# Kernel tuning notes

Measured on AMD Instinct MI355X. Metric: run time of the kernel, lower is better.

The kernel has to match this reference:

```python
import jax, jax.numpy as jnp
import numpy as np

EPS = 1e-5


def gcn_conv(x, src, dst, n_nodes, W, b):
    # x: [B, N, Fin]; src/dst: [E+N] (self loops included); W: [Fout, Fin]
    h = jnp.einsum('bnf,of->bno', x, W)                      # [B, N, Fout]
    deg = jnp.zeros((n_nodes,), h.dtype).at[dst].add(1.0)    # in-degree of A+I
    dinv = jnp.where(deg > 0, 1.0 / jnp.sqrt(deg), 0.0)
    norm = dinv[src] * dinv[dst]                             # [E+N]
    msg = h[:, src, :] * norm[None, :, None]                 # gather along node axis
    out = jnp.zeros_like(h).at[:, dst, :].add(msg)           # scatter-add aggregate
    return out + b


def batchnorm_nodes(x, gamma, beta):
    # torch BatchNorm1d(N) on [B, N, C]: channel axis is N, stats over (B, C)
    mean = jnp.mean(x, axis=(0, 2), keepdims=True)
    var = jnp.mean(jnp.square(x - mean), axis=(0, 2), keepdims=True)
    xn = (x - mean) * jax.lax.rsqrt(var + EPS)
    return xn * gamma[None, :, None] + beta[None, :, None]


def setup_inputs() -> dict:
    key = jax.random.key(0)
    ks = jax.random.split(key, 20)
    B, N, FIN, D, OUT, E = 4096, 64, 67, 2048, 2, 512
    s = 0.1
    d = {}
    d['x_fingerprints'] = jax.random.normal(ks[0], (B, D), jnp.float32)
    d['x_node_features'] = jax.random.normal(ks[1], (B, N, FIN), jnp.float32)
    d['edge_list'] = jax.random.randint(ks[2], (2, E), 0, N)
    d['W1'] = jax.random.normal(ks[3], (64, FIN), jnp.float32) * s
    d['b1'] = jax.random.normal(ks[4], (64,), jnp.float32) * s
    d['g1'] = 1.0 + jax.random.normal(ks[5], (N,), jnp.float32) * s
    d['be1'] = jax.random.normal(ks[6], (N,), jnp.float32) * s
    d['W2'] = jax.random.normal(ks[7], (32, 64), jnp.float32) * s
    d['b2'] = jax.random.normal(ks[8], (32,), jnp.float32) * s
    d['g2'] = 1.0 + jax.random.normal(ks[9], (N,), jnp.float32) * s
    d['be2'] = jax.random.normal(ks[10], (N,), jnp.float32) * s
    d['Wl1'] = jax.random.normal(ks[11], (400, D), jnp.float32) * (s / 4)
    d['bl1'] = jax.random.normal(ks[12], (400,), jnp.float32) * s
    d['Wl2'] = jax.random.normal(ks[13], (64, 400), jnp.float32) * s
    d['bl2'] = jax.random.normal(ks[14], (64,), jnp.float32) * s
    d['Wfc'] = jax.random.normal(ks[15], (OUT, 96), jnp.float32) * s
    d['bfc'] = jax.random.normal(ks[16], (OUT,), jnp.float32) * s
    return d


def reference(x_fingerprints, x_node_features, edge_list, W1, b1, g1, be1,
              W2, b2, g2, be2, Wl1, bl1, Wl2, bl2, Wfc, bfc):
    B, N, _ = x_node_features.shape
    loops = jnp.arange(N)
    src = jnp.concatenate([edge_list[0], loops])  # add self loops (GCNConv default)
    dst = jnp.concatenate([edge_list[1], loops])
    g = gcn_conv(x_node_features, src, dst, N, W1, b1)
    g = jax.nn.relu(batchnorm_nodes(g, g1, be1))
    g = gcn_conv(g, src, dst, N, W2, b2)
    g = jax.nn.relu(batchnorm_nodes(g, g2, be2))           # [B, N, 32]
    pooled = jnp.max(g, axis=1)                             # global_max_pool -> [B, 32]
    h = jax.nn.relu(x_fingerprints @ Wl1.T + bl1)
    h = jax.nn.relu(h @ Wl2.T + bl2)                        # [B, 64]
    out = jnp.concatenate([pooled, h], axis=1) @ Wfc.T + bfc
    return out
```

## Files before the change

### kernel.cpp

```cpp
#include <hip/hip_runtime.h>
#include <hip/hip_bf16.h>
#include <math.h>

typedef __bf16 bf16;
typedef __attribute__((ext_vector_type(8))) __bf16 bf16x8;
typedef __attribute__((ext_vector_type(4))) __bf16 bf16x4;
typedef __attribute__((ext_vector_type(4))) float f32x4;

#define EPSBN 1e-5f
#define NSLOT 128

__global__ __launch_bounds__(256) void k0_prep(const int* __restrict__ edge,
    const float* __restrict__ W1, const float* __restrict__ W2,
    float* __restrict__ partials,
    bf16* __restrict__ ahb,
    bf16* __restrict__ w1b,
    bf16* __restrict__ w2b)
{
    int tid = threadIdx.x;
    for (int i = blockIdx.x * 256 + tid; i < NSLOT * 64 * 4; i += gridDim.x * 256)
        partials[i] = 0.f;
    if (blockIdx.x == 1) {
        for (int i = tid; i < 64 * 104; i += 256) {
            int n = i / 104, f = i % 104;
            w1b[i] = (bf16)((f < 67) ? W1[n * 67 + f] : 0.f);
        }
        return;
    }
    if (blockIdx.x == 2) {
        for (int i = tid; i < 32 * 72; i += 256) {
            int n = i / 72, f = i % 72;
            w2b[i] = (bf16)((f < 64) ? W2[n * 64 + f] : 0.f);
        }
        return;
    }
    if (blockIdx.x != 0) return;

    __shared__ float Ah[64 * 64];
    __shared__ int deg[64];
    __shared__ float dinv[64];
    for (int i = tid; i < 4096; i += 256) Ah[i] = 0.f;
    if (tid < 64) deg[tid] = 1;
    __syncthreads();
    for (int e = tid; e < 512; e += 256) atomicAdd(&deg[edge[512 + e]], 1);
    __syncthreads();
    if (tid < 64) dinv[tid] = rsqrtf((float)deg[tid]);
    __syncthreads();
    for (int e = tid; e < 512; e += 256) {
        int s = edge[e], d = edge[512 + e];
        atomicAdd(&Ah[d * 64 + s], dinv[s] * dinv[d]);
    }
    if (tid < 64) atomicAdd(&Ah[tid * 64 + tid], dinv[tid] * dinv[tid]);
    __syncthreads();
    for (int i = tid; i < 64 * 72; i += 256) {
        int n = i / 72, s = i % 72;
        ahb[i] = (bf16)((s < 64) ? Ah[n * 64 + s] : 0.f);
    }
}

__global__ __launch_bounds__(256) void k1_gcn1(
    const float* __restrict__ x,
    const bf16* __restrict__ w1b,
    const bf16* __restrict__ ahb,
    const float* __restrict__ b1,
    bf16* __restrict__ g1out,
    float* __restrict__ part1)
{
    __shared__ bf16 sW[64 * 104];
    __shared__ bf16 sX[4 * 64 * 104];
    __shared__ bf16 sAh[64 * 72];
    __shared__ float sstat[128];
    int tid = threadIdx.x;
    int blk = blockIdx.x;
    if (tid < 128) sstat[tid] = 0.f;

#pragma unroll
    for (int k = 0; k < 4; ++k) {
        int c = tid + (k << 8);
        if (c < 832) ((bf16x8*)sW)[c] = ((const bf16x8*)w1b)[c];
    }
#pragma unroll
    for (int k = 0; k < 3; ++k) {
        int c = tid + (k << 8);
        if (c < 576) ((bf16x8*)sAh)[c] = ((const bf16x8*)ahb)[c];
    }
    const float* xb = x + (size_t)blk * 17152;
    for (int k = 0; k < 67; ++k) {
        int j = tid + (k << 8);
        int s = j / 4288, r = j % 4288;
        int n = r / 67, f = r % 67;
        sX[s * 6656 + n * 104 + f] = (bf16)xb[j];
    }
    for (int k = 0; k < 29; ++k) {
        int j = tid + (k << 8);
        int s = j / 1856, r = j % 1856;
        int n = r / 29, f = 67 + r % 29;
        sX[s * 6656 + n * 104 + f] = (bf16)0.f;
    }
    __syncthreads();

    int w = tid >> 6, lane = tid & 63, q = lane >> 4, r15 = lane & 15;
    bf16* myX = sX + w * 6656;
    f32x4 z4 = {0.f, 0.f, 0.f, 0.f};
    f32x4 acc[4][4];
#pragma unroll
    for (int mt = 0; mt < 4; ++mt)
#pragma unroll
        for (int nt = 0; nt < 4; ++nt) acc[mt][nt] = z4;
#pragma unroll
    for (int kt = 0; kt < 3; ++kt) {
        bf16x8 a_[4], b_[4];
#pragma unroll
        for (int mt = 0; mt < 4; ++mt)
            a_[mt] = *(const bf16x8*)&sW[(mt * 16 + r15) * 104 + kt * 32 + q * 8];
#pragma unroll
        for (int nt = 0; nt < 4; ++nt)
            b_[nt] = *(const bf16x8*)&myX[(nt * 16 + r15) * 104 + kt * 32 + q * 8];
#pragma unroll
        for (int mt = 0; mt < 4; ++mt)
#pragma unroll
            for (int nt = 0; nt < 4; ++nt)
                acc[mt][nt] = __builtin_amdgcn_mfma_f32_16x16x32_bf16(a_[mt], b_[nt], acc[mt][nt], 0, 0, 0);
    }
#pragma unroll
    for (int mt = 0; mt < 4; ++mt)
#pragma unroll
        for (int nt = 0; nt < 4; ++nt)
#pragma unroll
            for (int r = 0; r < 4; ++r)
                myX[(mt * 16 + q * 4 + r) * 104 + nt * 16 + r15] = (bf16)acc[mt][nt][r];

    bf16x8 ah[4][2], hb[4][2];
#pragma unroll
    for (int mt = 0; mt < 4; ++mt)
#pragma unroll
        for (int kt = 0; kt < 2; ++kt)
            ah[mt][kt] = *(const bf16x8*)&sAh[(mt * 16 + r15) * 72 + kt * 32 + q * 8];
#pragma unroll
    for (int ct = 0; ct < 4; ++ct)
#pragma unroll
        for (int kt = 0; kt < 2; ++kt)
            hb[ct][kt] = *(const bf16x8*)&myX[(ct * 16 + r15) * 104 + kt * 32 + q * 8];

    f32x4 o2[4][4];
#pragma unroll
    for (int mt = 0; mt < 4; ++mt)
#pragma unroll
        for (int ct = 0; ct < 4; ++ct) o2[mt][ct] = z4;
#pragma unroll
    for (int kt = 0; kt < 2; ++kt)
#pragma unroll
        for (int mt = 0; mt < 4; ++mt)
#pragma unroll
            for (int ct = 0; ct < 4; ++ct)
                o2[mt][ct] = __builtin_amdgcn_mfma_f32_16x16x32_bf16(ah[mt][kt], hb[ct][kt], o2[mt][ct], 0, 0, 0);

    float bv[4];
#pragma unroll
    for (int ct = 0; ct < 4; ++ct) bv[ct] = b1[ct * 16 + r15];
#pragma unroll
    for (int mt = 0; mt < 4; ++mt)
#pragma unroll
        for (int ct = 0; ct < 4; ++ct)
#pragma unroll
            for (int r = 0; r < 4; ++r)
                myX[(mt * 16 + q * 4 + r) * 72 + ct * 16 + r15] = (bf16)(o2[mt][ct][r] + bv[ct]);
    __syncthreads();

    bf16* gp = g1out + (size_t)blk * 16384;
#pragma unroll
    for (int k = 0; k < 8; ++k) {
        int c = tid + (k << 8);
        int s = c >> 9, rc = c & 511, n = rc >> 3, cc = rc & 7;
        bf16x8 v = *(const bf16x8*)&sX[s * 6656 + n * 72 + cc * 8];
        ((bf16x8*)gp)[c] = v;
        float s1 = 0.f, s2 = 0.f;
#pragma unroll
        for (int j = 0; j < 8; ++j) { float f = (float)v[j]; s1 += f; s2 += f * f; }
        atomicAdd(&sstat[n * 2 + 0], s1);
        atomicAdd(&sstat[n * 2 + 1], s2);
    }
    __syncthreads();
    if (tid < 64) {
        int slot = blk & (NSLOT - 1);
        atomicAdd(&part1[(slot * 64 + tid) * 2 + 0], sstat[tid * 2 + 0]);
        atomicAdd(&part1[(slot * 64 + tid) * 2 + 1], sstat[tid * 2 + 1]);
    }
}

__global__ __launch_bounds__(64) void k_bnstats(
    const float* __restrict__ part,
    const float* __restrict__ gamma, const float* __restrict__ beta,
    float* __restrict__ scale, float* __restrict__ shift, float inv_count)
{
    int n = blockIdx.x, t = threadIdx.x;
    float s1 = part[(t * 64 + n) * 2] + part[((t + 64) * 64 + n) * 2];
    float s2 = part[(t * 64 + n) * 2 + 1] + part[((t + 64) * 64 + n) * 2 + 1];
#pragma unroll
    for (int o = 32; o > 0; o >>= 1) { s1 += __shfl_down(s1, o); s2 += __shfl_down(s2, o); }
    if (t == 0) {
        float mean = s1 * inv_count;
        float var = s2 * inv_count - mean * mean;
        float sc = gamma[n] * rsqrtf(var + EPSBN);
        scale[n] = sc;
        shift[n] = beta[n] - mean * sc;
    }
}

__global__ __launch_bounds__(256) void k3_gcn2(
    const bf16* __restrict__ g1out,
    const bf16* __restrict__ w2b,
    const bf16* __restrict__ ahb,
    const float* __restrict__ b2,
    const float* __restrict__ scale1, const float* __restrict__ shift1,
    bf16* __restrict__ g2out,
    float* __restrict__ part2)
{
    __shared__ bf16 sW[32 * 72];
    __shared__ bf16 sY[4 * 64 * 72];
    __shared__ bf16 sAh[64 * 72];
    __shared__ float sstat[128];
    __shared__ float ssc[64], ssh[64];
    int tid = threadIdx.x;
    int blk = blockIdx.x;
    if (tid < 128) sstat[tid] = 0.f;
    if (tid < 64) { ssc[tid] = scale1[tid]; ssh[tid] = shift1[tid]; }
#pragma unroll
    for (int k = 0; k < 2; ++k) {
        int c = tid + (k << 8);
        if (c < 288) ((bf16x8*)sW)[c] = ((const bf16x8*)w2b)[c];
    }
#pragma unroll
    for (int k = 0; k < 3; ++k) {
        int c = tid + (k << 8);
        if (c < 576) ((bf16x8*)sAh)[c] = ((const bf16x8*)ahb)[c];
    }
    __syncthreads();

    const bf16* gb = g1out + (size_t)blk * 16384;
#pragma unroll
    for (int k = 0; k < 8; ++k) {
        int c = tid + (k << 8);
        int s = c >> 9, rc = c & 511, n = rc >> 3, cc = rc & 7;
        bf16x8 g = ((const bf16x8*)gb)[c];
        float sc = ssc[n], sh = ssh[n];
        bf16x8 y;
#pragma unroll
        for (int j = 0; j < 8; ++j)
            y[j] = (bf16)fmaxf(fmaf(sc, (float)g[j], sh), 0.f);
        *(bf16x8*)&sY[s * 4608 + n * 72 + cc * 8] = y;
    }
    __syncthreads();

    int w = tid >> 6, lane = tid & 63, q = lane >> 4, r15 = lane & 15;
    bf16* myY = sY + w * 4608;
    f32x4 z4 = {0.f, 0.f, 0.f, 0.f};
    f32x4 acc[2][4];
#pragma unroll
    for (int mt = 0; mt < 2; ++mt)
#pragma unroll
        for (int nt = 0; nt < 4; ++nt) acc[mt][nt] = z4;
#pragma unroll
    for (int kt = 0; kt < 2; ++kt) {
        bf16x8 a_[2], b_[4];
#pragma unroll
        for (int mt = 0; mt < 2; ++mt)
            a_[mt] = *(const bf16x8*)&sW[(mt * 16 + r15) * 72 + kt * 32 + q * 8];
#pragma unroll
        for (int nt = 0; nt < 4; ++nt)
            b_[nt] = *(const bf16x8*)&myY[(nt * 16 + r15) * 72 + kt * 32 + q * 8];
#pragma unroll
        for (int mt = 0; mt < 2; ++mt)
#pragma unroll
            for (int nt = 0; nt < 4; ++nt)
                acc[mt][nt] = __builtin_amdgcn_mfma_f32_16x16x32_bf16(a_[mt], b_[nt], acc[mt][nt], 0, 0, 0);
    }
#pragma unroll
    for (int mt = 0; mt < 2; ++mt)
#pragma unroll
        for (int nt = 0; nt < 4; ++nt)
#pragma unroll
            for (int r = 0; r < 4; ++r)
                myY[(mt * 16 + q * 4 + r) * 72 + nt * 16 + r15] = (bf16)acc[mt][nt][r];

    bf16x8 ah[4][2], hb[2][2];
#pragma unroll
    for (int mt = 0; mt < 4; ++mt)
#pragma unroll
        for (int kt = 0; kt < 2; ++kt)
            ah[mt][kt] = *(const bf16x8*)&sAh[(mt * 16 + r15) * 72 + kt * 32 + q * 8];
#pragma unroll
    for (int ct = 0; ct < 2; ++ct)
#pragma unroll
        for (int kt = 0; kt < 2; ++kt)
            hb[ct][kt] = *(const bf16x8*)&myY[(ct * 16 + r15) * 72 + kt * 32 + q * 8];

    f32x4 o2[4][2];
#pragma unroll
    for (int mt = 0; mt < 4; ++mt)
#pragma unroll
        for (int ct = 0; ct < 2; ++ct) o2[mt][ct] = z4;
#pragma unroll
    for (int kt = 0; kt < 2; ++kt)
#pragma unroll
        for (int mt = 0; mt < 4; ++mt)
#pragma unroll
            for (int ct = 0; ct < 2; ++ct)
                o2[mt][ct] = __builtin_amdgcn_mfma_f32_16x16x32_bf16(ah[mt][kt], hb[ct][kt], o2[mt][ct], 0, 0, 0);

    float bv[2];
#pragma unroll
    for (int ct = 0; ct < 2; ++ct) bv[ct] = b2[ct * 16 + r15];
#pragma unroll
    for (int mt = 0; mt < 4; ++mt)
#pragma unroll
        for (int ct = 0; ct < 2; ++ct)
#pragma unroll
            for (int r = 0; r < 4; ++r)
                myY[(mt * 16 + q * 4 + r) * 40 + ct * 16 + r15] = (bf16)(o2[mt][ct][r] + bv[ct]);
    __syncthreads();

    bf16* gp = g2out + (size_t)blk * 8192;
#pragma unroll
    for (int k = 0; k < 4; ++k) {
        int c = tid + (k << 8);
        int s = c >> 8, rc = c & 255, n = rc >> 2, cc = rc & 3;
        bf16x8 v = *(const bf16x8*)&sY[s * 4608 + n * 40 + cc * 8];
        ((bf16x8*)gp)[c] = v;
        float s1 = 0.f, s2 = 0.f;
#pragma unroll
        for (int j = 0; j < 8; ++j) { float f = (float)v[j]; s1 += f; s2 += f * f; }
        atomicAdd(&sstat[n * 2 + 0], s1);
        atomicAdd(&sstat[n * 2 + 1], s2);
    }
    __syncthreads();
    if (tid < 64) {
        int slot = blk & (NSLOT - 1);
        atomicAdd(&part2[(slot * 64 + tid) * 2 + 0], sstat[tid * 2 + 0]);
        atomicAdd(&part2[(slot * 64 + tid) * 2 + 1], sstat[tid * 2 + 1]);
    }
}

__global__ __launch_bounds__(256) void k6_mlp1(
    const float* __restrict__ A,
    const float* __restrict__ Bw,
    float* __restrict__ part)
{
    __shared__ bf16 As[64 * 36];
    __shared__ bf16 Bs[64 * 36];
    int tid = threadIdx.x;
    int m0 = blockIdx.x * 64, n0 = blockIdx.y * 64, ks = blockIdx.z;
    int row = tid >> 2, seg = tid & 3;
    int w = tid >> 6, lane = tid & 63, q = lane >> 4, r15 = lane & 15;
    f32x4 z4 = {0.f, 0.f, 0.f, 0.f};
    f32x4 acc[4] = {z4, z4, z4, z4};
    const float* pA = A + (size_t)(m0 + row) * 2048 + ks * 512 + seg * 8;
    bool bvalid = (n0 + row) < 400;
    const float* pB = Bw + (size_t)(n0 + row) * 2048 + ks * 512 + seg * 8;

    f32x4 a0 = *(const f32x4*)pA;
    f32x4 a1 = *(const f32x4*)(pA + 4);
    f32x4 c0 = z4, c1 = z4;
    if (bvalid) { c0 = *(const f32x4*)pB; c1 = *(const f32x4*)(pB + 4); }

    for (int kt = 0; kt < 16; ++kt) {
        bf16x8 apk, bpk;
        apk[0] = (bf16)a0[0]; apk[1] = (bf16)a0[1]; apk[2] = (bf16)a0[2]; apk[3] = (bf16)a0[3];
        apk[4] = (bf16)a1[0]; apk[5] = (bf16)a1[1]; apk[6] = (bf16)a1[2]; apk[7] = (bf16)a1[3];
        bpk[0] = (bf16)c0[0]; bpk[1] = (bf16)c0[1]; bpk[2] = (bf16)c0[2]; bpk[3] = (bf16)c0[3];
        bpk[4] = (bf16)c1[0]; bpk[5] = (bf16)c1[1]; bpk[6] = (bf16)c1[2]; bpk[7] = (bf16)c1[3];
        __syncthreads();
        *(bf16x8*)&As[row * 36 + seg * 8] = apk;
        *(bf16x8*)&Bs[row * 36 + seg * 8] = bpk;
        __syncthreads();
        if (kt < 15) {
            pA += 32; pB += 32;
            a0 = *(const f32x4*)pA; a1 = *(const f32x4*)(pA + 4);
            if (bvalid) { c0 = *(const f32x4*)pB; c1 = *(const f32x4*)(pB + 4); }
        }
        bf16x8 a = *(const bf16x8*)&As[(w * 16 + r15) * 36 + q * 8];
#pragma unroll
        for (int nt = 0; nt < 4; ++nt) {
            bf16x8 bb = *(const bf16x8*)&Bs[(nt * 16 + r15) * 36 + q * 8];
            acc[nt] = __builtin_amdgcn_mfma_f32_16x16x32_bf16(a, bb, acc[nt], 0, 0, 0);
        }
    }
    float* pp = part + (size_t)ks * 1638400;
#pragma unroll
    for (int nt = 0; nt < 4; ++nt)
#pragma unroll
        for (int r = 0; r < 4; ++r) {
            int mm = m0 + w * 16 + q * 4 + r;
            int nn = n0 + nt * 16 + r15;
            if (nn < 400) pp[(size_t)mm * 400 + nn] = acc[nt][r];
        }
}

__global__ __launch_bounds__(256) void k6_reduce(
    const float* __restrict__ part,
    const float* __restrict__ bias,
    bf16* __restrict__ h1)
{
    int i = blockIdx.x * 256 + threadIdx.x;
    const f32x4* p = (const f32x4*)part;
    f32x4 s0 = p[i], s1v = p[i + 409600], s2v = p[i + 819200], s3v = p[i + 1228800];
    int nn = (i * 4) % 400;
    f32x4 bv = *(const f32x4*)&bias[nn];
    bf16x4 ov;
    ov[0] = (bf16)fmaxf(s0[0] + s1v[0] + s2v[0] + s3v[0] + bv[0], 0.f);
    ov[1] = (bf16)fmaxf(s0[1] + s1v[1] + s2v[1] + s3v[1] + bv[1], 0.f);
    ov[2] = (bf16)fmaxf(s0[2] + s1v[2] + s2v[2] + s3v[2] + bv[2], 0.f);
    ov[3] = (bf16)fmaxf(s0[3] + s1v[3] + s2v[3] + s3v[3] + bv[3], 0.f);
    *(bf16x4*)&h1[i * 4] = ov;
}

__global__ __launch_bounds__(256) void k7_mlp2(
    const bf16* __restrict__ A,
    const float* __restrict__ Bw,
    const float* __restrict__ bias,
    float* __restrict__ Cout)
{
    __shared__ bf16 As[16 * 416];
    int tid = threadIdx.x;
    int m0 = blockIdx.x * 16;
    for (int i = tid; i < 16 * 50; i += 256) {
        int rr = i / 50, cc = (i % 50) * 8;
        *(bf16x8*)&As[rr * 416 + cc] = *(const bf16x8*)(A + (size_t)(m0 + rr) * 400 + cc);
    }
    if (tid < 32) {
        int rr = tid >> 1, cc = 400 + (tid & 1) * 8;
        bf16x8 z;
#pragma unroll
        for (int k = 0; k < 8; ++k) z[k] = (bf16)0.f;
        *(bf16x8*)&As[rr * 416 + cc] = z;
    }
    __syncthreads();

    int w = tid >> 6, lane = tid & 63, q = lane >> 4, r15 = lane & 15;
    f32x4 acc = {0.f, 0.f, 0.f, 0.f};
    const float* pB = Bw + (size_t)(w * 16 + r15) * 400;
#pragma unroll 4
    for (int kt = 0; kt < 13; ++kt) {
        int k0 = kt * 32 + q * 8;
        bf16x8 a = *(const bf16x8*)&As[r15 * 416 + k0];
        bf16x8 bb;
#pragma unroll
        for (int k = 0; k < 8; ++k) bb[k] = (bf16)0.f;
        if (k0 < 400) {
            f32x4 c0 = *(const f32x4*)(pB + k0);
            f32x4 c1 = *(const f32x4*)(pB + k0 + 4);
            bb[0] = (bf16)c0[0]; bb[1] = (bf16)c0[1]; bb[2] = (bf16)c0[2]; bb[3] = (bf16)c0[3];
            bb[4] = (bf16)c1[0]; bb[5] = (bf16)c1[1]; bb[6] = (bf16)c1[2]; bb[7] = (bf16)c1[3];
        }
        acc = __builtin_amdgcn_mfma_f32_16x16x32_bf16(a, bb, acc, 0, 0, 0);
    }
#pragma unroll
    for (int r = 0; r < 4; ++r) {
        int mm = m0 + q * 4 + r;
        int nn = w * 16 + r15;
        float v = fmaxf(acc[r] + bias[nn], 0.f);
        Cout[(size_t)mm * 64 + nn] = v;
    }
}

__global__ __launch_bounds__(256) void k8_final(
    const bf16* __restrict__ g2out,
    const float* __restrict__ scale2, const float* __restrict__ shift2,
    const float* __restrict__ h2,
    const float* __restrict__ Wfc,
    const float* __restrict__ bfc,
    float* __restrict__ out)
{
    __shared__ float s2s[64], sh2s[64];
    int tid = threadIdx.x;
    if (tid < 64) { s2s[tid] = scale2[tid]; sh2s[tid] = shift2[tid]; }
    __syncthreads();
    int w = tid >> 6, lane = tid & 63;
    int b = blockIdx.x * 4 + w;
    int c = lane & 31, half = lane >> 5;
    const bf16* gb = g2out + (size_t)b * 2048;
    float mx = 0.f;
    for (int i = 0; i < 32; ++i) {
        int n = half * 32 + i;
        float v = (float)gb[n * 32 + c];
        float val = fmaf(s2s[n], v, sh2s[n]);
        mx = fmaxf(mx, val);
    }
    mx = fmaxf(mx, __shfl_xor(mx, 32));
    float h2v = h2[(size_t)b * 64 + lane];
#pragma unroll
    for (int o = 0; o < 2; ++o) {
        float t = h2v * Wfc[o * 96 + 32 + lane];
        if (half == 0) t += mx * Wfc[o * 96 + c];
#pragma unroll
        for (int off = 32; off > 0; off >>= 1) t += __shfl_xor(t, off);
        if (lane == 0) out[(size_t)b * 2 + o] = t + bfc[o];
    }
}

extern "C" void kernel_launch(void* const* d_in, const int* in_sizes, int n_in,
                              void* d_out, int out_size, void* d_ws, size_t ws_size,
                              hipStream_t stream)
{
    const float* x_fp   = (const float*)d_in[0];
    const float* x_node = (const float*)d_in[1];
    const int*   edge   = (const int*)d_in[2];
    const float* W1     = (const float*)d_in[3];
    const float* b1     = (const float*)d_in[4];
    const float* g1     = (const float*)d_in[5];
    const float* be1    = (const float*)d_in[6];
    const float* W2     = (const float*)d_in[7];
    const float* b2     = (const float*)d_in[8];
    const float* g2     = (const float*)d_in[9];
    const float* be2    = (const float*)d_in[10];
    const float* Wl1    = (const float*)d_in[11];
    const float* bl1    = (const float*)d_in[12];
    const float* Wl2    = (const float*)d_in[13];
    const float* bl2    = (const float*)d_in[14];
    const float* Wfc    = (const float*)d_in[15];
    const float* bfc    = (const float*)d_in[16];
    float* out = (float*)d_out;

    char* ws = (char*)d_ws;
    bf16*  w1b     = (bf16*)(ws);
    bf16*  ahb     = (bf16*)(ws + 13312);
    bf16*  w2b     = (bf16*)(ws + 22528);
    float* scale1  = (float*)(ws + 27136);
    float* shift1  = (float*)(ws + 27392);
    float* scale2  = (float*)(ws + 27648);
    float* shift2  = (float*)(ws + 27904);
    float* part1   = (float*)(ws + 28672);
    float* part2   = (float*)(ws + 94208);
    bf16*  g1out   = (bf16*)(ws + 159744);
    float* part6   = (float*)(ws + 159744);
    bf16*  g2out   = (bf16*)(ws + 33714176ull);
    bf16*  h1      = (bf16*)(ws + 50491392ull);
    float* h2      = (float*)(ws + 53768192ull);

    k0_prep<<<dim3(16), dim3(256), 0, stream>>>(edge, W1, W2, part1, ahb, w1b, w2b);
    k1_gcn1<<<dim3(1024), dim3(256), 0, stream>>>(x_node, w1b, ahb, b1, g1out, part1);
    k_bnstats<<<dim3(64), dim3(64), 0, stream>>>(part1, g1, be1, scale1, shift1,
                                                 1.f / (4096.f * 64.f));
    k3_gcn2<<<dim3(1024), dim3(256), 0, stream>>>(g1out, w2b, ahb, b2, scale1, shift1,
                                                  g2out, part2);
    k_bnstats<<<dim3(64), dim3(64), 0, stream>>>(part2, g2, be2, scale2, shift2,
                                                 1.f / (4096.f * 32.f));
    k6_mlp1<<<dim3(64, 7, 4), dim3(256), 0, stream>>>(x_fp, Wl1, part6);
    k6_reduce<<<dim3(1600), dim3(256), 0, stream>>>(part6, bl1, h1);
    k7_mlp2<<<dim3(256), dim3(256), 0, stream>>>(h1, Wl2, bl2, h2);
    k8_final<<<dim3(1024), dim3(256), 0, stream>>>(g2out, scale2, shift2, h2, Wfc, bfc, out);
}
```

Measured before the change: 285.9 us.

## Pre-convert node features to padded bf16 and split GCN1 into chunked launches

Adds a conversion kernel that turns fp32 node features into a padded bf16 layout in quarter-batch chunks, each followed by a GCN1 launch. GCN1 now handles two samples per block, splitting each sample's work across two waves, and loads its tile with vector copies instead of scalar strided conversion. The aim is to remove the slow scattered fp32-to-bf16 staging and cut shared memory per block to raise occupancy. In exchange it adds an extra global round trip for the converted input, eight launches instead of one, and extra block barriers.

New measurement: 338.5 us. +18.4%, slower.

```diff
diff --git a/kernel.cpp b/kernel.cpp
--- a/kernel.cpp
+++ b/kernel.cpp
@@ -58,22 +58,50 @@
     }
 }
 
+__global__ __launch_bounds__(256) void kx_conv(const float* __restrict__ x,
+    bf16* __restrict__ xbq, int s0)
+{
+    int tid = threadIdx.x;
+    const float* xs = x + ((size_t)s0 + blockIdx.x * 2) * 4288;
+    bf16* xo = xbq + (size_t)blockIdx.x * 13312;
+#pragma unroll
+    for (int k = 0; k < 7; ++k) {
+        int c = tid + (k << 8);
+        if (c < 1664) {
+            int ls = c >> 9 >= 1 ? (c >= 832) : (c >= 832);
+            ls = (c >= 832) ? 1 : 0;
+            int cc = c - ls * 832;
+            int n = cc / 13;
+            int seg = cc - n * 13;
+            int f0 = seg * 8;
+            const float* src = xs + ls * 4288 + n * 67 + f0;
+            bf16x8 v;
+#pragma unroll
+            for (int j = 0; j < 8; ++j) {
+                float t = (f0 + j < 67) ? src[j] : 0.f;
+                v[j] = (bf16)t;
+            }
+            *(bf16x8*)(xo + (size_t)c * 8) = v;
+        }
+    }
+}
+
 __global__ __launch_bounds__(256) void k1_gcn1(
-    const float* __restrict__ x,
+    const bf16* __restrict__ xbq,
     const bf16* __restrict__ w1b,
     const bf16* __restrict__ ahb,
     const float* __restrict__ b1,
     bf16* __restrict__ g1out,
-    float* __restrict__ part1)
+    float* __restrict__ part1,
+    int s0)
 {
     __shared__ bf16 sW[64 * 104];
-    __shared__ bf16 sX[4 * 64 * 104];
+    __shared__ bf16 sX[2 * 64 * 104];
     __shared__ bf16 sAh[64 * 72];
     __shared__ float sstat[128];
     int tid = threadIdx.x;
     int blk = blockIdx.x;
     if (tid < 128) sstat[tid] = 0.f;
-
 #pragma unroll
     for (int k = 0; k < 4; ++k) {
         int c = tid + (k << 8);
@@ -84,73 +112,71 @@
         int c = tid + (k << 8);
         if (c < 576) ((bf16x8*)sAh)[c] = ((const bf16x8*)ahb)[c];
     }
-    const float* xb = x + (size_t)blk * 17152;
-    for (int k = 0; k < 67; ++k) {
-        int j = tid + (k << 8);
-        int s = j / 4288, r = j % 4288;
-        int n = r / 67, f = r % 67;
-        sX[s * 6656 + n * 104 + f] = (bf16)xb[j];
-    }
-    for (int k = 0; k < 29; ++k) {
-        int j = tid + (k << 8);
-        int s = j / 1856, r = j % 1856;
-        int n = r / 29, f = 67 + r % 29;
-        sX[s * 6656 + n * 104 + f] = (bf16)0.f;
+    const bf16x8* xp = (const bf16x8*)(xbq + (size_t)blk * 13312);
+#pragma unroll
+    for (int k = 0; k < 7; ++k) {
+        int c = tid + (k << 8);
+        if (c < 1664) ((bf16x8*)sX)[c] = xp[c];
     }
     __syncthreads();
 
     int w = tid >> 6, lane = tid & 63, q = lane >> 4, r15 = lane & 15;
-    bf16* myX = sX + w * 6656;
+    int sm = w >> 1, hw = w & 1;
+    bf16* myX = sX + sm * 6656;
     f32x4 z4 = {0.f, 0.f, 0.f, 0.f};
-    f32x4 acc[4][4];
-#pragma unroll
-    for (int mt = 0; mt < 4; ++mt)
+    f32x4 acc[2][4];
+#pragma unroll
+    for (int mt = 0; mt < 2; ++mt)
 #pragma unroll
         for (int nt = 0; nt < 4; ++nt) acc[mt][nt] = z4;
 #pragma unroll
     for (int kt = 0; kt < 3; ++kt) {
-        bf16x8 a_[4], b_[4];
-#pragma unroll
-        for (int mt = 0; mt < 4; ++mt)
-            a_[mt] = *(const bf16x8*)&sW[(mt * 16 + r15) * 104 + kt * 32 + q * 8];
+        bf16x8 a_[2], b_[4];
+#pragma unroll
+        for (int mt = 0; mt < 2; ++mt)
+            a_[mt] = *(const bf16x8*)&sW[((hw * 2 + mt) * 16 + r15) * 104 + kt * 32 + q * 8];
 #pragma unroll
         for (int nt = 0; nt < 4; ++nt)
             b_[nt] = *(const bf16x8*)&myX[(nt * 16 + r15) * 104 + kt * 32 + q * 8];
 #pragma unroll
-        for (int mt = 0; mt < 4; ++mt)
+        for (int mt = 0; mt < 2; ++mt)
 #pragma unroll
             for (int nt = 0; nt < 4; ++nt)
                 acc[mt][nt] = __builtin_amdgcn_mfma_f32_16x16x32_bf16(a_[mt], b_[nt], acc[mt][nt], 0, 0, 0);
     }
-#pragma unroll
-    for (int mt = 0; mt < 4; ++mt)
+    __syncthreads();
+#pragma unroll
+    for (int mt = 0; mt < 2; ++mt)
 #pragma unroll
         for (int nt = 0; nt < 4; ++nt)
 #pragma unroll
             for (int r = 0; r < 4; ++r)
-                myX[(mt * 16 + q * 4 + r) * 104 + nt * 16 + r15] = (bf16)acc[mt][nt][r];
-
-    bf16x8 ah[4][2], hb[4][2];
-#pragma unroll
-    for (int mt = 0; mt < 4; ++mt)
+                myX[((hw * 2 + mt) * 16 + q * 4 + r) * 104 + nt * 16 + r15] = (bf16)acc[mt][nt][r];
+
+    bf16x8 ah[2][2];
+#pragma unroll
+    for (int mt = 0; mt < 2; ++mt)
 #pragma unroll
         for (int kt = 0; kt < 2; ++kt)
-            ah[mt][kt] = *(const bf16x8*)&sAh[(mt * 16 + r15) * 72 + kt * 32 + q * 8];
+            ah[mt][kt] = *(const bf16x8*)&sAh[((hw * 2 + mt) * 16 + r15) * 72 + kt * 32 + q * 8];
+    __syncthreads();
+
+    bf16x8 hb[4][2];
 #pragma unroll
     for (int ct = 0; ct < 4; ++ct)
 #pragma unroll
         for (int kt = 0; kt < 2; ++kt)
             hb[ct][kt] = *(const bf16x8*)&myX[(ct * 16 + r15) * 104 + kt * 32 + q * 8];
 
-    f32x4 o2[4][4];
-#pragma unroll
-    for (int mt = 0; mt < 4; ++mt)
+    f32x4 o2[2][4];
+#pragma unroll
+    for (int mt = 0; mt < 2; ++mt)
 #pragma unroll
         for (int ct = 0; ct < 4; ++ct) o2[mt][ct] = z4;
 #pragma unroll
     for (int kt = 0; kt < 2; ++kt)
 #pragma unroll
-        for (int mt = 0; mt < 4; ++mt)
+        for (int mt = 0; mt < 2; ++mt)
 #pragma unroll
             for (int ct = 0; ct < 4; ++ct)
                 o2[mt][ct] = __builtin_amdgcn_mfma_f32_16x16x32_bf16(ah[mt][kt], hb[ct][kt], o2[mt][ct], 0, 0, 0);
@@ -158,18 +184,19 @@
     float bv[4];
 #pragma unroll
     for (int ct = 0; ct < 4; ++ct) bv[ct] = b1[ct * 16 + r15];
-#pragma unroll
-    for (int mt = 0; mt < 4; ++mt)
+    __syncthreads();
+#pragma unroll
+    for (int mt = 0; mt < 2; ++mt)
 #pragma unroll
         for (int ct = 0; ct < 4; ++ct)
 #pragma unroll
             for (int r = 0; r < 4; ++r)
-                myX[(mt * 16 + q * 4 + r) * 72 + ct * 16 + r15] = (bf16)(o2[mt][ct][r] + bv[ct]);
-    __syncthreads();
-
-    bf16* gp = g1out + (size_t)blk * 16384;
-#pragma unroll
-    for (int k = 0; k < 8; ++k) {
+                myX[((hw * 2 + mt) * 16 + q * 4 + r) * 72 + ct * 16 + r15] = (bf16)(o2[mt][ct][r] + bv[ct]);
+    __syncthreads();
+
+    bf16* gp = g1out + ((size_t)s0 + blk * 2) * 4096;
+#pragma unroll
+    for (int k = 0; k < 4; ++k) {
         int c = tid + (k << 8);
         int s = c >> 9, rc = c & 511, n = rc >> 3, cc = rc & 7;
         bf16x8 v = *(const bf16x8*)&sX[s * 6656 + n * 72 + cc * 8];
@@ -182,7 +209,7 @@
     }
     __syncthreads();
     if (tid < 64) {
-        int slot = blk & (NSLOT - 1);
+        int slot = (s0 + blk * 2) & (NSLOT - 1);
         atomicAdd(&part1[(slot * 64 + tid) * 2 + 0], sstat[tid * 2 + 0]);
         atomicAdd(&part1[(slot * 64 + tid) * 2 + 1], sstat[tid * 2 + 1]);
     }
@@ -531,14 +558,20 @@
     float* shift2  = (float*)(ws + 27904);
     float* part1   = (float*)(ws + 28672);
     float* part2   = (float*)(ws + 94208);
-    bf16*  g1out   = (bf16*)(ws + 159744);
-    float* part6   = (float*)(ws + 159744);
-    bf16*  g2out   = (bf16*)(ws + 33714176ull);
-    bf16*  h1      = (bf16*)(ws + 50491392ull);
-    float* h2      = (float*)(ws + 53768192ull);
+    char*  pool    = ws + 196608;
+    bf16*  g1out   = (bf16*)(pool);
+    float* part6   = (float*)(pool);
+    float* h2      = (float*)(pool + 26214400);
+    bf16*  xbq     = (bf16*)(pool + 33554432);
+    bf16*  g2out   = (bf16*)(pool + 33554432);
+    bf16*  h1      = (bf16*)(pool + 50331648);
 
     k0_prep<<<dim3(16), dim3(256), 0, stream>>>(edge, W1, W2, part1, ahb, w1b, w2b);
-    k1_gcn1<<<dim3(1024), dim3(256), 0, stream>>>(x_node, w1b, ahb, b1, g1out, part1);
+    for (int qtr = 0; qtr < 4; ++qtr) {
+        int s0 = qtr * 1024;
+        kx_conv<<<dim3(512), dim3(256), 0, stream>>>(x_node, xbq, s0);
+        k1_gcn1<<<dim3(512), dim3(256), 0, stream>>>(xbq, w1b, ahb, b1, g1out, part1, s0);
+    }
     k_bnstats<<<dim3(64), dim3(64), 0, stream>>>(part1, g1, be1, scale1, shift1,
                                                  1.f / (4096.f * 64.f));
     k3_gcn2<<<dim3(1024), dim3(256), 0, stream>>>(g1out, w2b, ahb, b2, scale1, shift1,
```

## Process one graph per block in GCN kernels, splitting matmul tiles across waves

Applied to the files above, without the earlier changes.

The two GCN kernels now handle a single graph per 256-thread block, with the four waves splitting the output row tiles, instead of each wave owning a whole graph. Grid size grows from 1024 to 4096 blocks. Weight and adjacency fragments are loaded straight from global memory into registers, and node features are staged with vectorized float4 loads before the bf16 conversion. The intent is to cut LDS use and register pressure for higher occupancy and better-coalesced input loads. The cost is more blocks, extra barriers between stages, and the workspace layout is rearranged so part6 no longer aliases g1out.

Measured after the change: 275.0 us. 3.8% less time.

```diff
diff --git a/kernel.cpp b/kernel.cpp
--- a/kernel.cpp
+++ b/kernel.cpp
@@ -66,113 +66,98 @@
     bf16* __restrict__ g1out,
     float* __restrict__ part1)
 {
-    __shared__ bf16 sW[64 * 104];
-    __shared__ bf16 sX[4 * 64 * 104];
-    __shared__ bf16 sAh[64 * 72];
+    __shared__ float sXf[4288];
+    __shared__ bf16 sX[64 * 104];
     __shared__ float sstat[128];
     int tid = threadIdx.x;
     int blk = blockIdx.x;
     if (tid < 128) sstat[tid] = 0.f;
 
-#pragma unroll
-    for (int k = 0; k < 4; ++k) {
+    const f32x4* xp = (const f32x4*)(x + (size_t)blk * 4288);
+#pragma unroll
+    for (int k = 0; k < 5; ++k) {
         int c = tid + (k << 8);
-        if (c < 832) ((bf16x8*)sW)[c] = ((const bf16x8*)w1b)[c];
-    }
-#pragma unroll
-    for (int k = 0; k < 3; ++k) {
+        if (c < 1072) ((f32x4*)sXf)[c] = xp[c];
+    }
+
+    int w = tid >> 6, lane = tid & 63, q = lane >> 4, r15 = lane & 15;
+    bf16x8 aw[3], ah[2];
+#pragma unroll
+    for (int kt = 0; kt < 3; ++kt)
+        aw[kt] = *(const bf16x8*)&w1b[(w * 16 + r15) * 104 + kt * 32 + q * 8];
+#pragma unroll
+    for (int kt = 0; kt < 2; ++kt)
+        ah[kt] = *(const bf16x8*)&ahb[(w * 16 + r15) * 72 + kt * 32 + q * 8];
+    __syncthreads();
+
+    {
+        int n = tid & 63, sg = tid >> 6;
+#pragma unroll
+        for (int i = 0; i < 4; ++i) {
+            int seg = sg + 4 * i;
+            if (seg < 13) {
+                int f0 = seg * 8;
+                bf16x8 v;
+#pragma unroll
+                for (int j = 0; j < 8; ++j) {
+                    int f = f0 + j;
+                    float t = (f < 67) ? sXf[n * 67 + f] : 0.f;
+                    v[j] = (bf16)t;
+                }
+                *(bf16x8*)&sX[n * 104 + f0] = v;
+            }
+        }
+    }
+    __syncthreads();
+
+    f32x4 z4 = {0.f, 0.f, 0.f, 0.f};
+    f32x4 acc[4] = {z4, z4, z4, z4};
+#pragma unroll
+    for (int kt = 0; kt < 3; ++kt) {
+        bf16x8 b_[4];
+#pragma unroll
+        for (int nt = 0; nt < 4; ++nt)
+            b_[nt] = *(const bf16x8*)&sX[(nt * 16 + r15) * 104 + kt * 32 + q * 8];
+#pragma unroll
+        for (int nt = 0; nt < 4; ++nt)
+            acc[nt] = __builtin_amdgcn_mfma_f32_16x16x32_bf16(aw[kt], b_[nt], acc[nt], 0, 0, 0);
+    }
+    __syncthreads();
+#pragma unroll
+    for (int nt = 0; nt < 4; ++nt)
+#pragma unroll
+        for (int r = 0; r < 4; ++r)
+            sX[(w * 16 + q * 4 + r) * 104 + nt * 16 + r15] = (bf16)acc[nt][r];
+    __syncthreads();
+
+    f32x4 o2[4] = {z4, z4, z4, z4};
+#pragma unroll
+    for (int kt = 0; kt < 2; ++kt) {
+        bf16x8 hbv[4];
+#pragma unroll
+        for (int ct = 0; ct < 4; ++ct)
+            hbv[ct] = *(const bf16x8*)&sX[(ct * 16 + r15) * 104 + kt * 32 + q * 8];
+#pragma unroll
+        for (int ct = 0; ct < 4; ++ct)
+            o2[ct] = __builtin_amdgcn_mfma_f32_16x16x32_bf16(ah[kt], hbv[ct], o2[ct], 0, 0, 0);
+    }
+    float bv[4];
+#pragma unroll
+    for (int ct = 0; ct < 4; ++ct) bv[ct] = b1[ct * 16 + r15];
+    __syncthreads();
+#pragma unroll
+    for (int ct = 0; ct < 4; ++ct)
+#pragma unroll
+        for (int r = 0; r < 4; ++r)
+            sX[(w * 16 + q * 4 + r) * 72 + ct * 16 + r15] = (bf16)(o2[ct][r] + bv[ct]);
+    __syncthreads();
+
+    bf16* gp = g1out + (size_t)blk * 4096;
+#pragma unroll
+    for (int k = 0; k < 2; ++k) {
         int c = tid + (k << 8);
-        if (c < 576) ((bf16x8*)sAh)[c] = ((const bf16x8*)ahb)[c];
-    }
-    const float* xb = x + (size_t)blk * 17152;
-    for (int k = 0; k < 67; ++k) {
-        int j = tid + (k << 8);
-        int s = j / 4288, r = j % 4288;
-        int n = r / 67, f = r % 67;
-        sX[s * 6656 + n * 104 + f] = (bf16)xb[j];
-    }
-    for (int k = 0; k < 29; ++k) {
-        int j = tid + (k << 8);
-        int s = j / 1856, r = j % 1856;
-        int n = r / 29, f = 67 + r % 29;
-        sX[s * 6656 + n * 104 + f] = (bf16)0.f;
-    }
-    __syncthreads();
-
-    int w = tid >> 6, lane = tid & 63, q = lane >> 4, r15 = lane & 15;
-    bf16* myX = sX + w * 6656;
-    f32x4 z4 = {0.f, 0.f, 0.f, 0.f};
-    f32x4 acc[4][4];
-#pragma unroll
-    for (int mt = 0; mt < 4; ++mt)
-#pragma unroll
-        for (int nt = 0; nt < 4; ++nt) acc[mt][nt] = z4;
-#pragma unroll
-    for (int kt = 0; kt < 3; ++kt) {
-        bf16x8 a_[4], b_[4];
-#pragma unroll
-        for (int mt = 0; mt < 4; ++mt)
-            a_[mt] = *(const bf16x8*)&sW[(mt * 16 + r15) * 104 + kt * 32 + q * 8];
-#pragma unroll
-        for (int nt = 0; nt < 4; ++nt)
-            b_[nt] = *(const bf16x8*)&myX[(nt * 16 + r15) * 104 + kt * 32 + q * 8];
-#pragma unroll
-        for (int mt = 0; mt < 4; ++mt)
-#pragma unroll
-            for (int nt = 0; nt < 4; ++nt)
-                acc[mt][nt] = __builtin_amdgcn_mfma_f32_16x16x32_bf16(a_[mt], b_[nt], acc[mt][nt], 0, 0, 0);
-    }
-#pragma unroll
-    for (int mt = 0; mt < 4; ++mt)
-#pragma unroll
-        for (int nt = 0; nt < 4; ++nt)
-#pragma unroll
-            for (int r = 0; r < 4; ++r)
-                myX[(mt * 16 + q * 4 + r) * 104 + nt * 16 + r15] = (bf16)acc[mt][nt][r];
-
-    bf16x8 ah[4][2], hb[4][2];
-#pragma unroll
-    for (int mt = 0; mt < 4; ++mt)
-#pragma unroll
-        for (int kt = 0; kt < 2; ++kt)
-            ah[mt][kt] = *(const bf16x8*)&sAh[(mt * 16 + r15) * 72 + kt * 32 + q * 8];
-#pragma unroll
-    for (int ct = 0; ct < 4; ++ct)
-#pragma unroll
-        for (int kt = 0; kt < 2; ++kt)
-            hb[ct][kt] = *(const bf16x8*)&myX[(ct * 16 + r15) * 104 + kt * 32 + q * 8];
-
-    f32x4 o2[4][4];
-#pragma unroll
-    for (int mt = 0; mt < 4; ++mt)
-#pragma unroll
-        for (int ct = 0; ct < 4; ++ct) o2[mt][ct] = z4;
-#pragma unroll
-    for (int kt = 0; kt < 2; ++kt)
-#pragma unroll
-        for (int mt = 0; mt < 4; ++mt)
-#pragma unroll
-            for (int ct = 0; ct < 4; ++ct)
-                o2[mt][ct] = __builtin_amdgcn_mfma_f32_16x16x32_bf16(ah[mt][kt], hb[ct][kt], o2[mt][ct], 0, 0, 0);
-
-    float bv[4];
-#pragma unroll
-    for (int ct = 0; ct < 4; ++ct) bv[ct] = b1[ct * 16 + r15];
-#pragma unroll
-    for (int mt = 0; mt < 4; ++mt)
-#pragma unroll
-        for (int ct = 0; ct < 4; ++ct)
-#pragma unroll
-            for (int r = 0; r < 4; ++r)
-                myX[(mt * 16 + q * 4 + r) * 72 + ct * 16 + r15] = (bf16)(o2[mt][ct][r] + bv[ct]);
-    __syncthreads();
-
-    bf16* gp = g1out + (size_t)blk * 16384;
-#pragma unroll
-    for (int k = 0; k < 8; ++k) {
-        int c = tid + (k << 8);
-        int s = c >> 9, rc = c & 511, n = rc >> 3, cc = rc & 7;
-        bf16x8 v = *(const bf16x8*)&sX[s * 6656 + n * 72 + cc * 8];
+        int n = c >> 3, cc = c & 7;
+        bf16x8 v = *(const bf16x8*)&sX[n * 72 + cc * 8];
         ((bf16x8*)gp)[c] = v;
         float s1 = 0.f, s2 = 0.f;
 #pragma unroll
@@ -216,116 +201,85 @@
     bf16* __restrict__ g2out,
     float* __restrict__ part2)
 {
-    __shared__ bf16 sW[32 * 72];
-    __shared__ bf16 sY[4 * 64 * 72];
-    __shared__ bf16 sAh[64 * 72];
+    __shared__ bf16 sY[64 * 72];
+    __shared__ bf16 sH[32 * 72];
+    __shared__ bf16 sO[64 * 40];
+    __shared__ float ssc[64], ssh[64];
     __shared__ float sstat[128];
-    __shared__ float ssc[64], ssh[64];
     int tid = threadIdx.x;
     int blk = blockIdx.x;
     if (tid < 128) sstat[tid] = 0.f;
     if (tid < 64) { ssc[tid] = scale1[tid]; ssh[tid] = shift1[tid]; }
+
+    int w = tid >> 6, lane = tid & 63, q = lane >> 4, r15 = lane & 15;
+    bf16x8 aw[2][2], ah[2];
+#pragma unroll
+    for (int mt = 0; mt < 2; ++mt)
+#pragma unroll
+        for (int kt = 0; kt < 2; ++kt)
+            aw[mt][kt] = *(const bf16x8*)&w2b[(mt * 16 + r15) * 72 + kt * 32 + q * 8];
+#pragma unroll
+    for (int kt = 0; kt < 2; ++kt)
+        ah[kt] = *(const bf16x8*)&ahb[(w * 16 + r15) * 72 + kt * 32 + q * 8];
+    __syncthreads();
+
+    const bf16* gb = g1out + (size_t)blk * 4096;
 #pragma unroll
     for (int k = 0; k < 2; ++k) {
         int c = tid + (k << 8);
-        if (c < 288) ((bf16x8*)sW)[c] = ((const bf16x8*)w2b)[c];
-    }
-#pragma unroll
-    for (int k = 0; k < 3; ++k) {
-        int c = tid + (k << 8);
-        if (c < 576) ((bf16x8*)sAh)[c] = ((const bf16x8*)ahb)[c];
-    }
-    __syncthreads();
-
-    const bf16* gb = g1out + (size_t)blk * 16384;
-#pragma unroll
-    for (int k = 0; k < 8; ++k) {
-        int c = tid + (k << 8);
-        int s = c >> 9, rc = c & 511, n = rc >> 3, cc = rc & 7;
+        int n = c >> 3, cc = c & 7;
         bf16x8 g = ((const bf16x8*)gb)[c];
         float sc = ssc[n], sh = ssh[n];
         bf16x8 y;
 #pragma unroll
         for (int j = 0; j < 8; ++j)
             y[j] = (bf16)fmaxf(fmaf(sc, (float)g[j], sh), 0.f);
-        *(bf16x8*)&sY[s * 4608 + n * 72 + cc * 8] = y;
-    }
-    __syncthreads();
-
-    int w = tid >> 6, lane = tid & 63, q = lane >> 4, r15 = lane & 15;
-    bf16* myY = sY + w * 4608;
+        *(bf16x8*)&sY[n * 72 + cc * 8] = y;
+    }
+    __syncthreads();
+
     f32x4 z4 = {0.f, 0.f, 0.f, 0.f};
-    f32x4 acc[2][4];
+    f32x4 acc[2] = {z4, z4};
+#pragma unroll
+    for (int kt = 0; kt < 2; ++kt) {
+        bf16x8 b_ = *(const bf16x8*)&sY[(w * 16 + r15) * 72 + kt * 32 + q * 8];
+#pragma unroll
+        for (int mt = 0; mt < 2; ++mt)
+            acc[mt] = __builtin_amdgcn_mfma_f32_16x16x32_bf16(aw[mt][kt], b_, acc[mt], 0, 0, 0);
+    }
 #pragma unroll
     for (int mt = 0; mt < 2; ++mt)
 #pragma unroll
-        for (int nt = 0; nt < 4; ++nt) acc[mt][nt] = z4;
+        for (int r = 0; r < 4; ++r)
+            sH[(mt * 16 + q * 4 + r) * 72 + w * 16 + r15] = (bf16)acc[mt][r];
+    __syncthreads();
+
+    f32x4 o2[2] = {z4, z4};
 #pragma unroll
     for (int kt = 0; kt < 2; ++kt) {
-        bf16x8 a_[2], b_[4];
-#pragma unroll
-        for (int mt = 0; mt < 2; ++mt)
-            a_[mt] = *(const bf16x8*)&sW[(mt * 16 + r15) * 72 + kt * 32 + q * 8];
-#pragma unroll
-        for (int nt = 0; nt < 4; ++nt)
-            b_[nt] = *(const bf16x8*)&myY[(nt * 16 + r15) * 72 + kt * 32 + q * 8];
-#pragma unroll
-        for (int mt = 0; mt < 2; ++mt)
-#pragma unroll
-            for (int nt = 0; nt < 4; ++nt)
-                acc[mt][nt] = __builtin_amdgcn_mfma_f32_16x16x32_bf16(a_[mt], b_[nt], acc[mt][nt], 0, 0, 0);
-    }
-#pragma unroll
-    for (int mt = 0; mt < 2; ++mt)
-#pragma unroll
-        for (int nt = 0; nt < 4; ++nt)
-#pragma unroll
-            for (int r = 0; r < 4; ++r)
-                myY[(mt * 16 + q * 4 + r) * 72 + nt * 16 + r15] = (bf16)acc[mt][nt][r];
-
-    bf16x8 ah[4][2], hb[2][2];
-#pragma unroll
-    for (int mt = 0; mt < 4; ++mt)
-#pragma unroll
-        for (int kt = 0; kt < 2; ++kt)
-            ah[mt][kt] = *(const bf16x8*)&sAh[(mt * 16 + r15) * 72 + kt * 32 + q * 8];
+        bf16x8 hbv[2];
+#pragma unroll
+        for (int ct = 0; ct < 2; ++ct)
+            hbv[ct] = *(const bf16x8*)&sH[(ct * 16 + r15) * 72 + kt * 32 + q * 8];
+#pragma unroll
+        for (int ct = 0; ct < 2; ++ct)
+            o2[ct] = __builtin_amdgcn_mfma_f32_16x16x32_bf16(ah[kt], hbv[ct], o2[ct], 0, 0, 0);
+    }
+    float bv[2];
+#pragma unroll
+    for (int ct = 0; ct < 2; ++ct) bv[ct] = b2[ct * 16 + r15];
 #pragma unroll
     for (int ct = 0; ct < 2; ++ct)
 #pragma unroll
-        for (int kt = 0; kt < 2; ++kt)
-            hb[ct][kt] = *(const bf16x8*)&myY[(ct * 16 + r15) * 72 + kt * 32 + q * 8];
-
-    f32x4 o2[4][2];
-#pragma unroll
-    for (int mt = 0; mt < 4; ++mt)
-#pragma unroll
-        for (int ct = 0; ct < 2; ++ct) o2[mt][ct] = z4;
-#pragma unroll
-    for (int kt = 0; kt < 2; ++kt)
-#pragma unroll
-        for (int mt = 0; mt < 4; ++mt)
-#pragma unroll
-            for (int ct = 0; ct < 2; ++ct)
-                o2[mt][ct] = __builtin_amdgcn_mfma_f32_16x16x32_bf16(ah[mt][kt], hb[ct][kt], o2[mt][ct], 0, 0, 0);
-
-    float bv[2];
-#pragma unroll
-    for (int ct = 0; ct < 2; ++ct) bv[ct] = b2[ct * 16 + r15];
-#pragma unroll
-    for (int mt = 0; mt < 4; ++mt)
-#pragma unroll
-        for (int ct = 0; ct < 2; ++ct)
-#pragma unroll
-            for (int r = 0; r < 4; ++r)
-                myY[(mt * 16 + q * 4 + r) * 40 + ct * 16 + r15] = (bf16)(o2[mt][ct][r] + bv[ct]);
-    __syncthreads();
-
-    bf16* gp = g2out + (size_t)blk * 8192;
-#pragma unroll
-    for (int k = 0; k < 4; ++k) {
-        int c = tid + (k << 8);
-        int s = c >> 8, rc = c & 255, n = rc >> 2, cc = rc & 3;
-        bf16x8 v = *(const bf16x8*)&sY[s * 4608 + n * 40 + cc * 8];
+        for (int r = 0; r < 4; ++r)
+            sO[(w * 16 + q * 4 + r) * 40 + ct * 16 + r15] = (bf16)(o2[ct][r] + bv[ct]);
+    __syncthreads();
+
+    bf16* gp = g2out + (size_t)blk * 2048;
+    {
+        int c = tid;
+        int n = c >> 2, cc = c & 3;
+        bf16x8 v = *(const bf16x8*)&sO[n * 40 + cc * 8];
         ((bf16x8*)gp)[c] = v;
         float s1 = 0.f, s2 = 0.f;
 #pragma unroll
@@ -531,17 +485,18 @@
     float* shift2  = (float*)(ws + 27904);
     float* part1   = (float*)(ws + 28672);
     float* part2   = (float*)(ws + 94208);
-    bf16*  g1out   = (bf16*)(ws + 159744);
-    float* part6   = (float*)(ws + 159744);
-    bf16*  g2out   = (bf16*)(ws + 33714176ull);
-    bf16*  h1      = (bf16*)(ws + 50491392ull);
-    float* h2      = (float*)(ws + 53768192ull);
+    char*  pool    = ws + 196608;
+    bf16*  g1out   = (bf16*)(pool);
+    bf16*  g2out   = (bf16*)(pool + 33554432ull);
+    float* part6   = (float*)(pool + 50331648ull);
+    bf16*  h1      = (bf16*)(pool + 76546048ull);
+    float* h2      = (float*)(pool + 79822848ull);
 
     k0_prep<<<dim3(16), dim3(256), 0, stream>>>(edge, W1, W2, part1, ahb, w1b, w2b);
-    k1_gcn1<<<dim3(1024), dim3(256), 0, stream>>>(x_node, w1b, ahb, b1, g1out, part1);
+    k1_gcn1<<<dim3(4096), dim3(256), 0, stream>>>(x_node, w1b, ahb, b1, g1out, part1);
     k_bnstats<<<dim3(64), dim3(64), 0, stream>>>(part1, g1, be1, scale1, shift1,
                                                  1.f / (4096.f * 64.f));
-    k3_gcn2<<<dim3(1024), dim3(256), 0, stream>>>(g1out, w2b, ahb, b2, scale1, shift1,
+    k3_gcn2<<<dim3(4096), dim3(256), 0, stream>>>(g1out, w2b, ahb, b2, scale1, shift1,
                                                   g2out, part2);
     k_bnstats<<<dim3(64), dim3(64), 0, stream>>>(part2, g2, be2, scale2, shift2,
                                                  1.f / (4096.f * 32.f));
```
